# Optimization experiments

Measured on AMD Instinct MI355X. Metric: run time of the kernel, lower is better.

The kernel has to match this reference:

```python
import jax, jax.numpy as jnp
import numpy as np

B, S, D = 2, 1024, 1024
E = 8          # routed experts
I = 1024       # per-expert intermediate
IS = 1024      # shared expert intermediate
TOP_K = 2
NUM_SHARED = 1


def setup_inputs() -> dict:
    key = jax.random.key(0)
    ks = jax.random.split(key, 8)
    scale = 0.02
    return {
        "x": jax.random.normal(ks[0], (B, S, D), dtype=jnp.float32),
        "w_gate": jax.random.normal(ks[1], (D, E), dtype=jnp.float32) * scale,
        "wg": jax.random.normal(ks[2], (E, D, I), dtype=jnp.float32) * scale,  # expert gate_proj
        "wu": jax.random.normal(ks[3], (E, D, I), dtype=jnp.float32) * scale,  # expert up_proj
        "wd": jax.random.normal(ks[4], (E, I, D), dtype=jnp.float32) * scale,  # expert down_proj
        "ws_g": jax.random.normal(ks[5], (NUM_SHARED, D, IS), dtype=jnp.float32) * scale,
        "ws_u": jax.random.normal(ks[6], (NUM_SHARED, D, IS), dtype=jnp.float32) * scale,
        "ws_d": jax.random.normal(ks[7], (NUM_SHARED, IS, D), dtype=jnp.float32) * scale,
    }


def _swiglu(t, w_gate_proj, w_up, w_down):
    # t: [N, D]
    g = t @ w_gate_proj            # [N, I]
    u = t @ w_up                   # [N, I]
    return (jax.nn.silu(g) * u) @ w_down  # [N, D]


def reference(x, w_gate, wg, wu, wd, ws_g, ws_u, ws_d):
    Bb, Ss, Dd = x.shape
    x_flat = x.reshape(Bb * Ss, Dd)                  # [N, D]
    N = x_flat.shape[0]

    # --- router ---
    logits = x_flat @ w_gate                          # [N, E]
    topk_logits, topk_idx = jax.lax.top_k(logits, TOP_K)
    topk_w = jax.nn.softmax(topk_logits, axis=-1)     # [N, K]

    # --- aux load-balancing loss ---
    one_hot = jax.nn.one_hot(topk_idx, E, dtype=jnp.float32)  # [N, K, E]
    f = one_hot.sum(axis=1).mean(axis=0)                       # [E]
    P = jax.nn.softmax(logits, axis=-1).mean(axis=0)           # [E]
    aux_loss = E * jnp.sum(f * P)

    # --- combine weights: cw[n, e] = sum_k topk_w[n,k] * 1[topk_idx[n,k]==e] ---
    cw = jnp.einsum("nk,nke->ne", topk_w, one_hot)             # [N, E]

    # --- routed experts: dense compute over all experts, weighted combine ---
    g = jnp.einsum("nd,edi->eni", x_flat, wg)                  # [E, N, I]
    u = jnp.einsum("nd,edi->eni", x_flat, wu)                  # [E, N, I]
    a = jax.nn.silu(g) * u                                     # [E, N, I]
    y = jnp.einsum("eni,eid->end", a, wd)                      # [E, N, D]
    routed = jnp.einsum("ne,end->nd", cw, y)                   # [N, D]

    # --- shared experts ---
    shared = jnp.zeros_like(x_flat)
    for s in range(NUM_SHARED):
        shared = shared + _swiglu(x_flat, ws_g[s], ws_u[s], ws_d[s])

    out = (routed + shared).reshape(Bb, Ss, Dd)
    return out, aux_loss
```

## Files before the change

### kernel.cpp

```cpp
#include <hip/hip_runtime.h>
#include <math.h>

typedef unsigned short u16;
typedef __attribute__((ext_vector_type(8))) short short8;
typedef __attribute__((ext_vector_type(4))) float f32x4;
typedef __attribute__((ext_vector_type(4))) unsigned short u16x4;
typedef __attribute__((ext_vector_type(8))) unsigned short u16x8;

#define N_TOK 2048
#define DIM 1024
#define OUT_ELEMS 2097152

#define GLDS16(gp, lp) __builtin_amdgcn_global_load_lds( \
    (const __attribute__((address_space(1))) unsigned int*)(gp), \
    (__attribute__((address_space(3))) unsigned int*)(lp), 16, 0, 0)

__device__ __forceinline__ u16 f2bf(float f) {
    union { float f; unsigned u; } v; v.f = f;
    unsigned r = (v.u + 0x7FFFu + ((v.u >> 16) & 1u)) >> 16;
    return (u16)r;
}
__device__ __forceinline__ float bf2f(u16 h) {
    union { unsigned u; float f; } v; v.u = ((unsigned)h) << 16;
    return v.f;
}

__global__ void k_init(int* __restrict__ tlist, int* __restrict__ curs,
                       float* __restrict__ Psum, int* __restrict__ cnt8) {
    int i = blockIdx.x * 256 + threadIdx.x;
    tlist[4096 + i] = i;
    if (i < 16) curs[i] = 0;
    if (i < 8) { Psum[i] = 0.f; cnt8[i] = 0; }
}

__global__ void k_cvt_w(const float* __restrict__ wg, const float* __restrict__ wu,
                        const float* __restrict__ wd, const float* __restrict__ wsg,
                        const float* __restrict__ wsu, const float* __restrict__ wsd,
                        u16* __restrict__ wgt, u16* __restrict__ wut,
                        u16* __restrict__ wdt, u16* __restrict__ wsgt,
                        u16* __restrict__ wsut, u16* __restrict__ wsdt) {
    __shared__ u16 tile[8 * 1024];
    int bx = blockIdx.x;
    int mat = bx >> 7;
    int chunk = bx & 127;
    const float* src; u16* dst;
    if      (mat <  8) { src = wg  + (size_t)mat * 1048576;        dst = wgt + (size_t)mat * 1048576; }
    else if (mat < 16) { src = wu  + (size_t)(mat - 8) * 1048576;  dst = wut + (size_t)(mat - 8) * 1048576; }
    else if (mat < 24) { src = wd  + (size_t)(mat - 16) * 1048576; dst = wdt + (size_t)(mat - 16) * 1048576; }
    else if (mat == 24){ src = wsg; dst = wsgt; }
    else if (mat == 25){ src = wsu; dst = wsut; }
    else               { src = wsd; dst = wsdt; }
    const float* srow = src + (size_t)chunk * 8192;
    u16* dchunk = dst + (size_t)chunk * 8192;
    int t = threadIdx.x;
    int r  = t >> 5;
    int c0 = (t & 31) * 4;
    f32x4 v[8];
#pragma unroll
    for (int j = 0; j < 8; j++)
        v[j] = *(const f32x4*)(srow + r * 1024 + c0 + j * 128);
#pragma unroll
    for (int j = 0; j < 8; j++) {
        u16x4 o;
        o.x = f2bf(v[j].x); o.y = f2bf(v[j].y); o.z = f2bf(v[j].z); o.w = f2bf(v[j].w);
        *(u16x4*)(tile + r * 1024 + c0 + j * 128) = o;
    }
    __syncthreads();
#pragma unroll
    for (int j = 0; j < 4; j++) {
        int n = t + j * 256;
        u16x8 o;
#pragma unroll
        for (int k = 0; k < 8; k++) o[k] = tile[k * 1024 + n];
        *(u16x8*)(dchunk + n * 8) = o;
    }
}

__global__ void k_router(const float* __restrict__ x, const float* __restrict__ wgate,
                         u16* __restrict__ xb, int* __restrict__ tidx,
                         float* __restrict__ tw, float* __restrict__ Psum,
                         int* __restrict__ cnt8) {
    __shared__ float sP[8];
    __shared__ int   sC[8];
    int t = threadIdx.x;
    if (t < 8) { sP[t] = 0.f; sC[t] = 0; }
    __syncthreads();
    int wave = t >> 6;
    int lane = t & 63;
    int n = blockIdx.x * 4 + wave;
    const float* xr = x + (size_t)n * DIM;
    u16* xbr = xb + (size_t)n * DIM;
    float acc[8] = {0.f,0.f,0.f,0.f,0.f,0.f,0.f,0.f};
#pragma unroll
    for (int i = 0; i < 16; i++) {
        int d = lane + i * 64;
        float xv = xr[d];
        xbr[d] = f2bf(xv);
        const float* wr = wgate + d * 8;
#pragma unroll
        for (int e = 0; e < 8; e++) acc[e] += xv * wr[e];
    }
#pragma unroll
    for (int off = 32; off; off >>= 1) {
#pragma unroll
        for (int e = 0; e < 8; e++) acc[e] += __shfl_xor(acc[e], off);
    }
    if (lane == 0) {
        float mx = acc[0];
#pragma unroll
        for (int e = 1; e < 8; e++) mx = fmaxf(mx, acc[e]);
        float p[8], s = 0.f;
#pragma unroll
        for (int e = 0; e < 8; e++) { p[e] = expf(acc[e] - mx); s += p[e]; }
        float inv = 1.f / s;
#pragma unroll
        for (int e = 0; e < 8; e++) atomicAdd(&sP[e], p[e] * inv);
        int i0 = 0; float b0 = acc[0];
#pragma unroll
        for (int e = 1; e < 8; e++) if (acc[e] > b0) { b0 = acc[e]; i0 = e; }
        int i1 = -1; float b1 = -3.4e38f;
#pragma unroll
        for (int e = 0; e < 8; e++) if (e != i0 && acc[e] > b1) { b1 = acc[e]; i1 = e; }
        float w0 = 1.f / (1.f + expf(b1 - b0));
        tidx[n * 2] = i0; tidx[n * 2 + 1] = i1;
        tw[n * 2] = w0;   tw[n * 2 + 1] = 1.f - w0;
        atomicAdd(&sC[i0], 1);
        atomicAdd(&sC[i1], 1);
    }
    __syncthreads();
    if (t < 8) {
        atomicAdd(&Psum[t], sP[t]);
        atomicAdd(&cnt8[t], sC[t]);
    }
}

__global__ void k_scatter(const int* __restrict__ tidx, const float* __restrict__ Psum,
                          const int* __restrict__ cnt8, int* __restrict__ curs,
                          int* __restrict__ tlist, int* __restrict__ slots,
                          float* __restrict__ out, int* __restrict__ counts,
                          int* __restrict__ offs) {
    __shared__ int s_off[8];
    int t = threadIdx.x;
    if (t == 0) {
        int o = 0;
        for (int e = 0; e < 8; e++) { s_off[e] = o; o += cnt8[e]; }
    }
    __syncthreads();
    if (blockIdx.x == 0 && t == 0) {
        float aux = 0.f;
        for (int e = 0; e < 8; e++) {
            int c = cnt8[e];
            aux += (float)c * Psum[e];
            offs[e] = s_off[e]; counts[e] = c;
        }
        out[OUT_ELEMS] = 8.f * aux / ((float)N_TOK * (float)N_TOK);
        offs[8] = 4096; counts[8] = 2048;
    }
    int n = blockIdx.x * 256 + t;
    if (n < N_TOK) {
#pragma unroll
        for (int k = 0; k < 2; k++) {
            int e = tidx[n * 2 + k];
            int p = atomicAdd(&curs[e], 1);
            int sl = s_off[e] + p;
            tlist[sl] = n;
            slots[n * 2 + k] = sl;
        }
    }
}

__global__ __launch_bounds__(256, 2)
void k_gemm1(const u16* __restrict__ xb, const u16* __restrict__ wgt,
             const u16* __restrict__ wut, const u16* __restrict__ wsgt,
             const u16* __restrict__ wsut, const int* __restrict__ tlist,
             const int* __restrict__ counts, const int* __restrict__ offs,
             u16* __restrict__ H) {
    int bx = blockIdx.x;
    int job = bx >> 7;
    int mt = (bx >> 3) & 15;
    int nt = bx & 7;
    int jcnt = counts[job];
    int m0 = mt << 7;
    if (m0 >= jcnt) return;
    int joff = offs[job];
    int n0 = nt << 7;
    const u16* Bg = (job < 8) ? (wgt + (size_t)job * 1048576) : wsgt;
    const u16* Bu = (job < 8) ? (wut + (size_t)job * 1048576) : wsut;

    __shared__ __attribute__((aligned(128))) u16 As[4096];
    __shared__ __attribute__((aligned(128))) u16 Bgs[4096];
    __shared__ __attribute__((aligned(128))) u16 Bus[4096];

    int t = threadIdx.x;
    int wave = t >> 6, lane = t & 63;
    int ch = (lane & 3) * 8;
    int r0 = (wave * 2 + 0) * 16 + (lane >> 2);
    int r1 = (wave * 2 + 1) * 16 + (lane >> 2);
    int tok0 = tlist[joff + m0 + r0];
    int tok1 = tlist[joff + m0 + r1];
    const u16* a0 = xb + (size_t)tok0 * 1024 + ch;
    const u16* a1 = xb + (size_t)tok1 * 1024 + ch;
    const u16* gB = Bg + (size_t)wave * 8192 + (size_t)(n0 + lane) * 8;
    const u16* uB = Bu + (size_t)wave * 8192 + (size_t)(n0 + lane) * 8;
    u16* lA0 = As  + (wave * 2 + 0) * 512;  u16* lA1 = As  + (wave * 2 + 1) * 512;
    u16* lGa = Bgs + wave * 1024;           u16* lGb = Bgs + wave * 1024 + 512;
    u16* lUa = Bus + wave * 1024;           u16* lUb = Bus + wave * 1024 + 512;

    int wm = (wave >> 1) << 6, wn = (wave & 1) << 6;
    int quad = lane >> 4, lr = lane & 15;

    f32x4 accg[4][4], accu[4][4];
    f32x4 zz = {0.f, 0.f, 0.f, 0.f};
#pragma unroll
    for (int i = 0; i < 4; i++)
#pragma unroll
        for (int j = 0; j < 4; j++) { accg[i][j] = zz; accu[i][j] = zz; }

    for (int k0 = 0; k0 < 1024; k0 += 32) {
        size_t koff = (size_t)k0 * 1024;
        GLDS16(a0 + k0, lA0);        GLDS16(a1 + k0, lA1);
        GLDS16(gB + koff, lGa);      GLDS16(gB + koff + 512, lGb);
        GLDS16(uB + koff, lUa);      GLDS16(uB + koff + 512, lUb);
        __syncthreads();
        short8 af[4], bgf[4], buf[4];
#pragma unroll
        for (int i = 0; i < 4; i++) {
            int nrow = wn + i * 16 + lr;
            af[i]  = *(const short8*)(As  + (wm + i * 16 + lr) * 32 + quad * 8);
            bgf[i] = *(const short8*)(Bgs + quad * 1024 + nrow * 8);
            buf[i] = *(const short8*)(Bus + quad * 1024 + nrow * 8);
        }
#pragma unroll
        for (int mi = 0; mi < 4; mi++)
#pragma unroll
            for (int ni = 0; ni < 4; ni++) {
                accg[mi][ni] = __builtin_amdgcn_mfma_f32_16x16x32_bf16(af[mi], bgf[ni], accg[mi][ni], 0, 0, 0);
                accu[mi][ni] = __builtin_amdgcn_mfma_f32_16x16x32_bf16(af[mi], buf[ni], accu[mi][ni], 0, 0, 0);
            }
        __syncthreads();
    }
#pragma unroll
    for (int mi = 0; mi < 4; mi++) {
        int rowb = m0 + wm + mi * 16 + quad * 4;
#pragma unroll
        for (int rr = 0; rr < 4; rr++) {
            int row = rowb + rr;
            if (row < jcnt) {
                size_t base = (size_t)(joff + row) * 1024 + n0 + wn;
#pragma unroll
                for (int ni = 0; ni < 4; ni++) {
                    float g = accg[mi][ni][rr];
                    float u = accu[mi][ni][rr];
                    float h = (g / (1.f + expf(-g))) * u;
                    H[base + ni * 16 + lr] = f2bf(h);
                }
            }
        }
    }
}

__global__ __launch_bounds__(256, 2)
void k_gemm2(const u16* __restrict__ H, const u16* __restrict__ wdt,
             const u16* __restrict__ wsdt, const int* __restrict__ counts,
             const int* __restrict__ offs, u16* __restrict__ Y) {
    int bx = blockIdx.x;
    int job = bx >> 7;
    int mt = (bx >> 3) & 15;
    int nt = bx & 7;
    int jcnt = counts[job];
    int m0 = mt << 7;
    if (m0 >= jcnt) return;
    int joff = offs[job];
    int n0 = nt << 7;
    const u16* Bt = (job < 8) ? (wdt + (size_t)job * 1048576) : wsdt;

    __shared__ __attribute__((aligned(128))) u16 As[4096];
    __shared__ __attribute__((aligned(128))) u16 Bs[4096];

    int t = threadIdx.x;
    int wave = t >> 6, lane = t & 63;
    int ch = (lane & 3) * 8;
    int r0 = (wave * 2 + 0) * 16 + (lane >> 2);
    int r1 = (wave * 2 + 1) * 16 + (lane >> 2);
    const u16* a0 = H + (size_t)(joff + m0 + r0) * 1024 + ch;
    const u16* a1 = H + (size_t)(joff + m0 + r1) * 1024 + ch;
    const u16* bB = Bt + (size_t)wave * 8192 + (size_t)(n0 + lane) * 8;
    u16* lA0 = As + (wave * 2 + 0) * 512;  u16* lA1 = As + (wave * 2 + 1) * 512;
    u16* lBa = Bs + wave * 1024;           u16* lBb = Bs + wave * 1024 + 512;

    int wm = (wave >> 1) << 6, wn = (wave & 1) << 6;
    int quad = lane >> 4, lr = lane & 15;

    f32x4 acc[4][4];
    f32x4 zz = {0.f, 0.f, 0.f, 0.f};
#pragma unroll
    for (int i = 0; i < 4; i++)
#pragma unroll
        for (int j = 0; j < 4; j++) acc[i][j] = zz;

    for (int k0 = 0; k0 < 1024; k0 += 32) {
        size_t koff = (size_t)k0 * 1024;
        GLDS16(a0 + k0, lA0);    GLDS16(a1 + k0, lA1);
        GLDS16(bB + koff, lBa);  GLDS16(bB + koff + 512, lBb);
        __syncthreads();
        short8 af[4], bf[4];
#pragma unroll
        for (int i = 0; i < 4; i++) {
            af[i] = *(const short8*)(As + (wm + i * 16 + lr) * 32 + quad * 8);
            bf[i] = *(const short8*)(Bs + quad * 1024 + (wn + i * 16 + lr) * 8);
        }
#pragma unroll
        for (int mi = 0; mi < 4; mi++)
#pragma unroll
            for (int ni = 0; ni < 4; ni++)
                acc[mi][ni] = __builtin_amdgcn_mfma_f32_16x16x32_bf16(af[mi], bf[ni], acc[mi][ni], 0, 0, 0);
        __syncthreads();
    }
#pragma unroll
    for (int mi = 0; mi < 4; mi++) {
        int rowb = m0 + wm + mi * 16 + quad * 4;
#pragma unroll
        for (int rr = 0; rr < 4; rr++) {
            int row = rowb + rr;
            if (row < jcnt) {
                u16* yrow = Y + (size_t)(joff + row) * 1024 + n0 + wn;
#pragma unroll
                for (int ni = 0; ni < 4; ni++)
                    yrow[ni * 16 + lr] = f2bf(acc[mi][ni][rr]);
            }
        }
    }
}

__global__ void k_combine(const u16* __restrict__ Y, const int* __restrict__ slots,
                          const float* __restrict__ tw, float* __restrict__ out) {
    int n = blockIdx.x;
    int d = threadIdx.x;
    int s0 = slots[n * 2], s1 = slots[n * 2 + 1];
    float w0 = tw[n * 2], w1 = tw[n * 2 + 1];
    u16x4 y0 = ((const u16x4*)(Y + (size_t)s0 * 1024))[d];
    u16x4 y1 = ((const u16x4*)(Y + (size_t)s1 * 1024))[d];
    u16x4 ys = ((const u16x4*)(Y + (size_t)(4096 + n) * 1024))[d];
    f32x4 r;
    r.x = w0 * bf2f(y0.x) + w1 * bf2f(y1.x) + bf2f(ys.x);
    r.y = w0 * bf2f(y0.y) + w1 * bf2f(y1.y) + bf2f(ys.y);
    r.z = w0 * bf2f(y0.z) + w1 * bf2f(y1.z) + bf2f(ys.z);
    r.w = w0 * bf2f(y0.w) + w1 * bf2f(y1.w) + bf2f(ys.w);
    ((f32x4*)(out + (size_t)n * 1024))[d] = r;
}

extern "C" void kernel_launch(void* const* d_in, const int* in_sizes, int n_in,
                              void* d_out, int out_size, void* d_ws, size_t ws_size,
                              hipStream_t stream) {
    const float* x     = (const float*)d_in[0];
    const float* wgate = (const float*)d_in[1];
    const float* wg    = (const float*)d_in[2];
    const float* wu    = (const float*)d_in[3];
    const float* wd    = (const float*)d_in[4];
    const float* wsg   = (const float*)d_in[5];
    const float* wsu   = (const float*)d_in[6];
    const float* wsd   = (const float*)d_in[7];
    float* out = (float*)d_out;

    char* ws = (char*)d_ws;
    u16*   xb    = (u16*)(ws + 0);
    u16*   wgt   = (u16*)(ws + 4194304);
    u16*   wut   = (u16*)(ws + 20971520);
    u16*   wdt   = (u16*)(ws + 37748736);
    u16*   wsgt  = (u16*)(ws + 54525952);
    u16*   wsut  = (u16*)(ws + 56623104);
    u16*   wsdt  = (u16*)(ws + 58720256);
    u16*   H     = (u16*)(ws + 60817408);
    u16*   Y     = (u16*)(ws + 4194304);
    int*   tidx  = (int*)(ws + 73400320);
    float* tw    = (float*)(ws + 73416704);
    int*   tlist = (int*)(ws + 73433088);
    int*   slots = (int*)(ws + 73457664);
    int*   counts= (int*)(ws + 73474048);
    int*   offs  = (int*)(ws + 73474112);
    int*   curs  = (int*)(ws + 73474176);
    float* Psum  = (float*)(ws + 73474240);
    int*   cnt8  = (int*)(ws + 73474304);

    k_init<<<8, 256, 0, stream>>>(tlist, curs, Psum, cnt8);
    k_router<<<512, 256, 0, stream>>>(x, wgate, xb, tidx, tw, Psum, cnt8);
    k_scatter<<<8, 256, 0, stream>>>(tidx, Psum, cnt8, curs, tlist, slots,
                                     out, counts, offs);
    k_cvt_w<<<3456, 256, 0, stream>>>(wg, wu, wd, wsg, wsu, wsd,
                                      wgt, wut, wdt, wsgt, wsut, wsdt);
    k_gemm1<<<1152, 256, 0, stream>>>(xb, wgt, wut, wsgt, wsut, tlist, counts, offs, H);
    k_gemm2<<<1152, 256, 0, stream>>>(H, wdt, wsdt, counts, offs, Y);
    k_combine<<<2048, 256, 0, stream>>>(Y, slots, tw, out);
}
```

Measured before the change: 271.3 us.

## Double-buffer LDS tiles in both expert GEMM kernels to overlap loads with MFMA

Both grouped GEMM kernels now use two LDS buffers per operand and issue the async global-to-LDS loads for the next K step before computing on the current one. This halves the barriers per K step and is meant to hide global load latency behind the MFMA work. The cost is double the LDS footprint: 48KB per block for gemm1, which may reduce occupancy. Correctness depends on the compiler's waitcnt before each barrier covering the in-flight async LDS loads.

```diff
diff --git a/kernel.cpp b/kernel.cpp
--- a/kernel.cpp
+++ b/kernel.cpp
@@ -187,24 +187,21 @@
     const u16* Bg = (job < 8) ? (wgt + (size_t)job * 1048576) : wsgt;
     const u16* Bu = (job < 8) ? (wut + (size_t)job * 1048576) : wsut;
 
-    __shared__ __attribute__((aligned(128))) u16 As[4096];
-    __shared__ __attribute__((aligned(128))) u16 Bgs[4096];
-    __shared__ __attribute__((aligned(128))) u16 Bus[4096];
+    __shared__ __attribute__((aligned(128))) u16 As[8192];
+    __shared__ __attribute__((aligned(128))) u16 Bgs[8192];
+    __shared__ __attribute__((aligned(128))) u16 Bus[8192];
 
     int t = threadIdx.x;
     int wave = t >> 6, lane = t & 63;
     int ch = (lane & 3) * 8;
-    int r0 = (wave * 2 + 0) * 16 + (lane >> 2);
-    int r1 = (wave * 2 + 1) * 16 + (lane >> 2);
+    int r0 = (wave * 2) * 16 + (lane >> 2);
+    int r1 = r0 + 16;
     int tok0 = tlist[joff + m0 + r0];
     int tok1 = tlist[joff + m0 + r1];
     const u16* a0 = xb + (size_t)tok0 * 1024 + ch;
     const u16* a1 = xb + (size_t)tok1 * 1024 + ch;
     const u16* gB = Bg + (size_t)wave * 8192 + (size_t)(n0 + lane) * 8;
     const u16* uB = Bu + (size_t)wave * 8192 + (size_t)(n0 + lane) * 8;
-    u16* lA0 = As  + (wave * 2 + 0) * 512;  u16* lA1 = As  + (wave * 2 + 1) * 512;
-    u16* lGa = Bgs + wave * 1024;           u16* lGb = Bgs + wave * 1024 + 512;
-    u16* lUa = Bus + wave * 1024;           u16* lUb = Bus + wave * 1024 + 512;
 
     int wm = (wave >> 1) << 6, wn = (wave & 1) << 6;
     int quad = lane >> 4, lr = lane & 15;
@@ -216,29 +213,50 @@
 #pragma unroll
         for (int j = 0; j < 4; j++) { accg[i][j] = zz; accu[i][j] = zz; }
 
-    for (int k0 = 0; k0 < 1024; k0 += 32) {
-        size_t koff = (size_t)k0 * 1024;
-        GLDS16(a0 + k0, lA0);        GLDS16(a1 + k0, lA1);
-        GLDS16(gB + koff, lGa);      GLDS16(gB + koff + 512, lGb);
-        GLDS16(uB + koff, lUa);      GLDS16(uB + koff + 512, lUb);
-        __syncthreads();
-        short8 af[4], bgf[4], buf[4];
+    auto stage = [&](int bo, int step) {
+        int k0 = step * 32;
+        size_t koff = (size_t)step * 32768;
+        GLDS16(a0 + k0, As + bo + (wave * 2) * 512);
+        GLDS16(a1 + k0, As + bo + (wave * 2 + 1) * 512);
+        GLDS16(gB + koff,       Bgs + bo + wave * 1024);
+        GLDS16(gB + koff + 512, Bgs + bo + wave * 1024 + 512);
+        GLDS16(uB + koff,       Bus + bo + wave * 1024);
+        GLDS16(uB + koff + 512, Bus + bo + wave * 1024 + 512);
+    };
+    auto compute = [&](int bo) {
+        short8 af[4], bgf[4], bff[4];
 #pragma unroll
         for (int i = 0; i < 4; i++) {
             int nrow = wn + i * 16 + lr;
-            af[i]  = *(const short8*)(As  + (wm + i * 16 + lr) * 32 + quad * 8);
-            bgf[i] = *(const short8*)(Bgs + quad * 1024 + nrow * 8);
-            buf[i] = *(const short8*)(Bus + quad * 1024 + nrow * 8);
+            af[i]  = *(const short8*)(As  + bo + (wm + i * 16 + lr) * 32 + quad * 8);
+            bgf[i] = *(const short8*)(Bgs + bo + quad * 1024 + nrow * 8);
+            bff[i] = *(const short8*)(Bus + bo + quad * 1024 + nrow * 8);
         }
 #pragma unroll
         for (int mi = 0; mi < 4; mi++)
 #pragma unroll
             for (int ni = 0; ni < 4; ni++) {
                 accg[mi][ni] = __builtin_amdgcn_mfma_f32_16x16x32_bf16(af[mi], bgf[ni], accg[mi][ni], 0, 0, 0);
-                accu[mi][ni] = __builtin_amdgcn_mfma_f32_16x16x32_bf16(af[mi], buf[ni], accu[mi][ni], 0, 0, 0);
+                accu[mi][ni] = __builtin_amdgcn_mfma_f32_16x16x32_bf16(af[mi], bff[ni], accu[mi][ni], 0, 0, 0);
             }
+    };
+
+    stage(0, 0);
+#pragma unroll 1
+    for (int s = 0; s < 15; s++) {
         __syncthreads();
-    }
+        stage(4096, 2 * s + 1);
+        compute(0);
+        __syncthreads();
+        stage(0, 2 * s + 2);
+        compute(4096);
+    }
+    __syncthreads();
+    stage(4096, 31);
+    compute(0);
+    __syncthreads();
+    compute(4096);
+
 #pragma unroll
     for (int mi = 0; mi < 4; mi++) {
         int rowb = m0 + wm + mi * 16 + quad * 4;
@@ -274,19 +292,17 @@
     int n0 = nt << 7;
     const u16* Bt = (job < 8) ? (wdt + (size_t)job * 1048576) : wsdt;
 
-    __shared__ __attribute__((aligned(128))) u16 As[4096];
-    __shared__ __attribute__((aligned(128))) u16 Bs[4096];
+    __shared__ __attribute__((aligned(128))) u16 As[8192];
+    __shared__ __attribute__((aligned(128))) u16 Bs[8192];
 
     int t = threadIdx.x;
     int wave = t >> 6, lane = t & 63;
     int ch = (lane & 3) * 8;
-    int r0 = (wave * 2 + 0) * 16 + (lane >> 2);
-    int r1 = (wave * 2 + 1) * 16 + (lane >> 2);
+    int r0 = (wave * 2) * 16 + (lane >> 2);
+    int r1 = r0 + 16;
     const u16* a0 = H + (size_t)(joff + m0 + r0) * 1024 + ch;
     const u16* a1 = H + (size_t)(joff + m0 + r1) * 1024 + ch;
     const u16* bB = Bt + (size_t)wave * 8192 + (size_t)(n0 + lane) * 8;
-    u16* lA0 = As + (wave * 2 + 0) * 512;  u16* lA1 = As + (wave * 2 + 1) * 512;
-    u16* lBa = Bs + wave * 1024;           u16* lBb = Bs + wave * 1024 + 512;
 
     int wm = (wave >> 1) << 6, wn = (wave & 1) << 6;
     int quad = lane >> 4, lr = lane & 15;
@@ -298,24 +314,44 @@
 #pragma unroll
         for (int j = 0; j < 4; j++) acc[i][j] = zz;
 
-    for (int k0 = 0; k0 < 1024; k0 += 32) {
-        size_t koff = (size_t)k0 * 1024;
-        GLDS16(a0 + k0, lA0);    GLDS16(a1 + k0, lA1);
-        GLDS16(bB + koff, lBa);  GLDS16(bB + koff + 512, lBb);
-        __syncthreads();
+    auto stage = [&](int bo, int step) {
+        int k0 = step * 32;
+        size_t koff = (size_t)step * 32768;
+        GLDS16(a0 + k0, As + bo + (wave * 2) * 512);
+        GLDS16(a1 + k0, As + bo + (wave * 2 + 1) * 512);
+        GLDS16(bB + koff,       Bs + bo + wave * 1024);
+        GLDS16(bB + koff + 512, Bs + bo + wave * 1024 + 512);
+    };
+    auto compute = [&](int bo) {
         short8 af[4], bf[4];
 #pragma unroll
         for (int i = 0; i < 4; i++) {
-            af[i] = *(const short8*)(As + (wm + i * 16 + lr) * 32 + quad * 8);
-            bf[i] = *(const short8*)(Bs + quad * 1024 + (wn + i * 16 + lr) * 8);
+            af[i] = *(const short8*)(As + bo + (wm + i * 16 + lr) * 32 + quad * 8);
+            bf[i] = *(const short8*)(Bs + bo + quad * 1024 + (wn + i * 16 + lr) * 8);
         }
 #pragma unroll
         for (int mi = 0; mi < 4; mi++)
 #pragma unroll
             for (int ni = 0; ni < 4; ni++)
                 acc[mi][ni] = __builtin_amdgcn_mfma_f32_16x16x32_bf16(af[mi], bf[ni], acc[mi][ni], 0, 0, 0);
+    };
+
+    stage(0, 0);
+#pragma unroll 1
+    for (int s = 0; s < 15; s++) {
         __syncthreads();
-    }
+        stage(4096, 2 * s + 1);
+        compute(0);
+        __syncthreads();
+        stage(0, 2 * s + 2);
+        compute(4096);
+    }
+    __syncthreads();
+    stage(4096, 31);
+    compute(0);
+    __syncthreads();
+    compute(4096);
+
 #pragma unroll
     for (int mi = 0; mi < 4; mi++) {
         int rowb = m0 + wm + mi * 16 + quad * 4;
```

Result: no change. 276.1 us (+1.8%).
